# Kernel tuning notes

Hardware: AMD Instinct MI355X
Metric: run time of the kernel (lower is better)

The kernel has to match this reference:

```python
import jax, jax.numpy as jnp
import numpy as np

N, L, H, Q = 64, 258, 1024, 256
WINDOW = 16.0
DEV_POW = 128.0  # 2 * (window/2)^2, Luong local-p sigma = D/2


def setup_inputs() -> dict:
    key = jax.random.key(0)
    k1, k2, k3, k4, k5, k6 = jax.random.split(key, 6)
    encoder_outputs = jax.random.normal(k1, (N, L, H), dtype=jnp.float32)
    decoder_h_t = jax.random.normal(k2, (N, Q, H), dtype=jnp.float32)
    src_len = jax.random.randint(k3, (N,), 32, L + 1).astype(jnp.int32)
    # window centers within each source sentence
    p_t = jax.random.uniform(k4, (N,), dtype=jnp.float32) * (src_len.astype(jnp.float32) - 1.0)
    W_a = jax.random.normal(k5, (H, H), dtype=jnp.float32) * (1.0 / np.sqrt(H))
    W_c = jax.random.normal(k6, (H, 2 * H), dtype=jnp.float32) * (1.0 / np.sqrt(2 * H))
    return {"encoder_outputs": encoder_outputs, "decoder_h_t": decoder_h_t,
            "src_len": src_len, "p_t": p_t, "W_a": W_a, "W_c": W_c}


def reference(encoder_outputs, decoder_h_t, src_len, p_t, W_a, W_c):
    n, l, h = encoder_outputs.shape
    idx = jnp.arange(l, dtype=jnp.float32)  # index_matrix, length == max_length == L

    # local_p window: [p_t - D, p_t + D], clamped to [0, src_len]
    src_end = src_len.astype(jnp.float32)
    attn_start = jnp.maximum(p_t - WINDOW, 0.0)          # [N]
    attn_end = jnp.minimum(p_t + WINDOW, src_end)        # [N]
    mask = (idx[None, :] < attn_start[:, None]) | (idx[None, :] > attn_end[:, None])  # [N,L]

    # Luong 'general' score: h_t^T W_a h_s -> [N,Q,L]
    score = jnp.einsum('nqh,hk,nlk->nql', decoder_h_t, W_a, encoder_outputs)

    score = jnp.where(mask[:, None, :], -1e9, score)
    align = jax.nn.softmax(score, axis=2)                 # [N,Q,L]

    # gaussian reweighting centered at p_t
    gauss = jnp.exp(-((idx[None, :] - p_t[:, None]) ** 2) / DEV_POW)  # [N,L]
    align = align * gauss[:, None, :]

    context = jnp.einsum('nql,nlh->nqh', align, encoder_outputs)      # [N,Q,H]
    cat = jnp.concatenate([context, decoder_h_t], axis=2)             # [N,Q,2H]
    return jnp.tanh(cat @ W_c.T)                                      # [N,Q,H]
```

## Files before the change

kernel.cpp:

```cpp
#include <hip/hip_runtime.h>
#include <hip/hip_bf16.h>
#include <cstdint>

#define DEVINL __device__ __forceinline__

typedef __attribute__((ext_vector_type(8))) short short8;
typedef __attribute__((ext_vector_type(4))) float f32x4;
typedef __attribute__((ext_vector_type(4))) unsigned short u16x4;

static constexpr int NB = 64, LL = 258, HH = 1024, QQ = 256;
static constexpr int WROWS = 33;
static constexpr int MU = 2176;
static constexpr int VTN = 4096;

static constexpr size_t OFF_META = 0;
static constexpr size_t SZ_WE   = (size_t)MU * HH * 2;
static constexpr size_t OFF_WEHI = 1024;
static constexpr size_t OFF_WELO = OFF_WEHI + SZ_WE;
static constexpr size_t OFF_WAHI = OFF_WELO + SZ_WE;
static constexpr size_t OFF_WALO = OFF_WAHI + (size_t)HH * HH * 2;
static constexpr size_t OFF_WCBF = OFF_WALO + (size_t)HH * HH * 2;
static constexpr size_t OFF_HBF  = OFF_WCBF + (size_t)HH * 2 * HH * 2;
static constexpr size_t OFF_U    = OFF_HBF + (size_t)NB * QQ * HH * 2;
static constexpr size_t OFF_UHI  = OFF_U;
static constexpr size_t OFF_ULO  = OFF_U + (size_t)MU * HH * 2;
static constexpr size_t OFF_CTX  = OFF_U + (size_t)MU * HH * 4;
static constexpr size_t OFF_VT   = OFF_CTX + (size_t)NB * QQ * HH * 2;

DEVINL unsigned short f2bf(float x) {
    union { float f; uint32_t u; } v; v.f = x;
    uint32_t u = v.u;
    uint32_t r = (u + 0x7FFFu + ((u >> 16) & 1u)) >> 16;
    return (unsigned short)r;
}
DEVINL float bf2f(unsigned short b) {
    union { uint32_t u; float f; } v; v.u = ((uint32_t)b) << 16;
    return v.f;
}

template <typename T>
DEVINL void lds_load16(const T* g, T* l) {
    __builtin_amdgcn_global_load_lds(
        (const __attribute__((address_space(1))) void*)g,
        (__attribute__((address_space(3))) void*)l, 16, 0, 0);
}

DEVINL float fast_tanh(float x) {
    float e = __expf(2.0f * x);
    return 1.0f - 2.0f / (e + 1.0f);
}

DEVINL void window_of(float p, int sl, int& ls, int& lc) {
    float se = (float)sl;
    float s = fmaxf(p - 16.0f, 0.0f);
    float e = fminf(p + 16.0f, se);
    ls = (int)ceilf(s);
    int le = (int)floorf(e); if (le > LL - 1) le = LL - 1;
    lc = le - ls + 1;
    if (lc < 0) lc = 0;
    if (lc > WROWS) lc = WROWS;
}

__global__ __launch_bounds__(256) void k_prep(const float* __restrict__ enc,
                                              const float* __restrict__ ht,
                                              const float* __restrict__ pt,
                                              const int* __restrict__ slen,
                                              const float* __restrict__ Wa,
                                              const float* __restrict__ Wc,
                                              unsigned short* __restrict__ wehi,
                                              unsigned short* __restrict__ welo,
                                              unsigned short* __restrict__ wahi,
                                              unsigned short* __restrict__ walo,
                                              unsigned short* __restrict__ wcbf,
                                              unsigned short* __restrict__ hbf) {
    const int b = blockIdx.x, t = threadIdx.x;
    if (b < MU) {
        int r = b;
        const float* src = nullptr;
        bool valid = false;
        if (r < NB * WROWS) {
            int n = r / WROWS, li = r - n * WROWS;
            int ls, lc;
            window_of(pt[n], slen[n], ls, lc);
            if (li < lc) { valid = true; src = enc + ((size_t)n * LL + ls + li) * HH; }
        }
        f32x4 v;
        if (valid) v = ((const f32x4*)src)[t];
        else { v[0] = 0.f; v[1] = 0.f; v[2] = 0.f; v[3] = 0.f; }
        u16x4 h, l;
#pragma unroll
        for (int j = 0; j < 4; ++j) {
            unsigned short hb = f2bf(v[j]);
            h[j] = hb;
            l[j] = f2bf(v[j] - bf2f(hb));
        }
        size_t o = (size_t)r * HH / 4 + t;
        ((u16x4*)wehi)[o] = h;
        ((u16x4*)welo)[o] = l;
    } else if (b < MU + 1024) {
        int i = (b - MU) * 256 + t;
        f32x4 v = ((const f32x4*)Wa)[i];
        u16x4 h, l;
#pragma unroll
        for (int j = 0; j < 4; ++j) {
            unsigned short hb = f2bf(v[j]);
            h[j] = hb;
            l[j] = f2bf(v[j] - bf2f(hb));
        }
        ((u16x4*)wahi)[i] = h;
        ((u16x4*)walo)[i] = l;
    } else if (b < MU + 1024 + 2048) {
        int i = (b - MU - 1024) * 256 + t;
        f32x4 v = ((const f32x4*)Wc)[i];
        u16x4 h;
#pragma unroll
        for (int j = 0; j < 4; ++j) h[j] = f2bf(v[j]);
        ((u16x4*)wcbf)[i] = h;
    } else {
        int i = (b - MU - 3072) * 256 + t;
        f32x4 v = ((const f32x4*)ht)[i];
        u16x4 h;
#pragma unroll
        for (int j = 0; j < 4; ++j) h[j] = f2bf(v[j]);
        ((u16x4*)hbf)[i] = h;
    }
}

__global__ __launch_bounds__(256) void k_ugemm64(const unsigned short* __restrict__ Ahi,
                                                 const unsigned short* __restrict__ Alo,
                                                 const unsigned short* __restrict__ Bhi,
                                                 const unsigned short* __restrict__ Blo,
                                                 unsigned short* __restrict__ Uhi,
                                                 unsigned short* __restrict__ Ulo) {
    __shared__ unsigned short sAh[2][64 * 32], sAl[2][64 * 32], sBh[2][64 * 32], sBl[2][64 * 32];
    const int tid = threadIdx.x;
    const int w = tid >> 6, lane = tid & 63;
    const int m0 = blockIdx.y * 64, n0 = blockIdx.x * 64;
    const int wr = w >> 1, wc = w & 1;
    const int r16 = lane & 15, khalf = lane >> 4;
    const int srow = tid >> 2;
    const int scol = ((tid & 3) ^ ((tid >> 3) & 3)) * 8;
    const int ldso = tid * 8;
    const int kslot = (khalf ^ ((r16 >> 1) & 3)) * 8;
    f32x4 acc[2][2] = {};

    auto stage = [&](int buf, int kb) {
        lds_load16(Ahi + (size_t)(m0 + srow) * HH + kb + scol, &sAh[buf][ldso]);
        lds_load16(Alo + (size_t)(m0 + srow) * HH + kb + scol, &sAl[buf][ldso]);
        lds_load16(Bhi + (size_t)(n0 + srow) * HH + kb + scol, &sBh[buf][ldso]);
        lds_load16(Blo + (size_t)(n0 + srow) * HH + kb + scol, &sBl[buf][ldso]);
    };

    stage(0, 0);
    for (int t = 0; t < 32; ++t) {
        const int buf = t & 1;
        asm volatile("s_waitcnt vmcnt(0)" ::: "memory");
        __builtin_amdgcn_s_barrier();
        short8 ah[2], al[2], bh[2], bl[2];
#pragma unroll
        for (int f = 0; f < 2; ++f) {
            int ai = (wr * 32 + f * 16 + r16) * 32 + kslot;
            ah[f] = *(const short8*)&sAh[buf][ai];
            al[f] = *(const short8*)&sAl[buf][ai];
            int bi = (wc * 32 + f * 16 + r16) * 32 + kslot;
            bh[f] = *(const short8*)&sBh[buf][bi];
            bl[f] = *(const short8*)&sBl[buf][bi];
        }
        if (t + 1 < 32) stage(buf ^ 1, (t + 1) * 32);
        asm volatile("s_waitcnt lgkmcnt(0)" ::: "memory");
        __builtin_amdgcn_sched_barrier(0);
#pragma unroll
        for (int mf = 0; mf < 2; ++mf)
#pragma unroll
            for (int nf = 0; nf < 2; ++nf) {
                acc[mf][nf] = __builtin_amdgcn_mfma_f32_16x16x32_bf16(ah[mf], bh[nf], acc[mf][nf], 0, 0, 0);
                acc[mf][nf] = __builtin_amdgcn_mfma_f32_16x16x32_bf16(ah[mf], bl[nf], acc[mf][nf], 0, 0, 0);
                acc[mf][nf] = __builtin_amdgcn_mfma_f32_16x16x32_bf16(al[mf], bh[nf], acc[mf][nf], 0, 0, 0);
            }
        __builtin_amdgcn_s_barrier();
    }
    const int rg = lane >> 4;
#pragma unroll
    for (int mf = 0; mf < 2; ++mf)
#pragma unroll
        for (int nf = 0; nf < 2; ++nf)
#pragma unroll
            for (int r = 0; r < 4; ++r) {
                int m = m0 + wr * 32 + mf * 16 + rg * 4 + r;
                int nn = n0 + wc * 32 + nf * 16 + r16;
                float v = acc[mf][nf][r];
                unsigned short h = f2bf(v);
                Uhi[(size_t)m * HH + nn] = h;
                Ulo[(size_t)m * HH + nn] = f2bf(v - bf2f(h));
            }
}

__global__ __launch_bounds__(256) void k_vgemm64(const unsigned short* __restrict__ Wc1,
                                                 const unsigned short* __restrict__ Bhi,
                                                 const unsigned short* __restrict__ Blo,
                                                 unsigned short* __restrict__ VT) {
    __shared__ unsigned short sA[2][64 * 32], sBh[2][64 * 32], sBl[2][64 * 32];
    const int tid = threadIdx.x;
    const int w = tid >> 6, lane = tid & 63;
    const int m0 = blockIdx.y * 64, n0 = blockIdx.x * 64;
    const int wr = w >> 1, wc = w & 1;
    const int r16 = lane & 15, khalf = lane >> 4;
    const int srow = tid >> 2;
    const int scol = ((tid & 3) ^ ((tid >> 3) & 3)) * 8;
    const int ldso = tid * 8;
    const int kslot = (khalf ^ ((r16 >> 1) & 3)) * 8;
    f32x4 acc[2][2] = {};

    auto stage = [&](int buf, int kb) {
        lds_load16(Wc1 + (size_t)(m0 + srow) * (2 * HH) + kb + scol, &sA[buf][ldso]);
        lds_load16(Bhi + (size_t)(n0 + srow) * HH + kb + scol, &sBh[buf][ldso]);
        lds_load16(Blo + (size_t)(n0 + srow) * HH + kb + scol, &sBl[buf][ldso]);
    };

    stage(0, 0);
    for (int t = 0; t < 32; ++t) {
        const int buf = t & 1;
        asm volatile("s_waitcnt vmcnt(0)" ::: "memory");
        __builtin_amdgcn_s_barrier();
        short8 af[2], bh[2], bl[2];
#pragma unroll
        for (int f = 0; f < 2; ++f) {
            af[f] = *(const short8*)&sA[buf][(wr * 32 + f * 16 + r16) * 32 + kslot];
            int bi = (wc * 32 + f * 16 + r16) * 32 + kslot;
            bh[f] = *(const short8*)&sBh[buf][bi];
            bl[f] = *(const short8*)&sBl[buf][bi];
        }
        if (t + 1 < 32) stage(buf ^ 1, (t + 1) * 32);
        asm volatile("s_waitcnt lgkmcnt(0)" ::: "memory");
        __builtin_amdgcn_sched_barrier(0);
#pragma unroll
        for (int mf = 0; mf < 2; ++mf)
#pragma unroll
            for (int nf = 0; nf < 2; ++nf) {
                acc[mf][nf] = __builtin_amdgcn_mfma_f32_16x16x32_bf16(af[mf], bh[nf], acc[mf][nf], 0, 0, 0);
                acc[mf][nf] = __builtin_amdgcn_mfma_f32_16x16x32_bf16(af[mf], bl[nf], acc[mf][nf], 0, 0, 0);
            }
        __builtin_amdgcn_s_barrier();
    }
    const int rg = lane >> 4;
#pragma unroll
    for (int mf = 0; mf < 2; ++mf)
#pragma unroll
        for (int nf = 0; nf < 2; ++nf)
#pragma unroll
            for (int r = 0; r < 4; ++r) {
                int o = m0 + wr * 32 + mf * 16 + rg * 4 + r;
                int wrow = n0 + wc * 32 + nf * 16 + r16;
                int n = wrow / WROWS, li = wrow - n * WROWS;
                if (n < NB)
                    VT[(size_t)o * VTN + n * 64 + li] = f2bf(acc[mf][nf][r]);
            }
}

__global__ __launch_bounds__(256) void k_attn2(const float* __restrict__ ht,
                                               const unsigned short* __restrict__ Uhi,
                                               const unsigned short* __restrict__ Ulo,
                                               const unsigned short* __restrict__ VT,
                                               const float* __restrict__ pt,
                                               const int* __restrict__ slen,
                                               unsigned short* __restrict__ ctxP) {
    __shared__ float sPart[4][32 * 48];
    __shared__ float sScore[32 * 48];
    __shared__ unsigned short sPhi[32 * 72];
    __shared__ unsigned short sPlo[32 * 72];

    const int tid = threadIdx.x;
    const int w = tid >> 6, lane = tid & 63;
    const int n = blockIdx.x >> 3, q0 = (blockIdx.x & 7) * 32;
    int ls, lc;
    window_of(pt[n], slen[n], ls, lc);
    const float p = pt[n];
    const int r16 = lane & 15, khalf = lane >> 4, rg = lane >> 4;

    const float* hbase = ht + ((size_t)(n * QQ + q0)) * HH;
    const unsigned short* uhbase = Uhi + (size_t)n * WROWS * HH;
    const unsigned short* ulbase = Ulo + (size_t)n * WROWS * HH;

    f32x4 acc[2][3] = {};
    for (int ks = 0; ks < 8; ++ks) {
        int kcol = w * 256 + ks * 32 + khalf * 8;
        short8 ah[2], al[2];
#pragma unroll
        for (int mf = 0; mf < 2; ++mf) {
            const float* src = hbase + (size_t)(mf * 16 + r16) * HH + kcol;
            f32x4 v0 = *(const f32x4*)src;
            f32x4 v1 = *(const f32x4*)(src + 4);
            float vv[8] = {v0[0], v0[1], v0[2], v0[3], v1[0], v1[1], v1[2], v1[3]};
#pragma unroll
            for (int j = 0; j < 8; ++j) {
                unsigned short hb = f2bf(vv[j]);
                ah[mf][j] = (short)hb;
                al[mf][j] = (short)f2bf(vv[j] - bf2f(hb));
            }
        }
#pragma unroll
        for (int nf = 0; nf < 3; ++nf) {
            size_t uoff = (size_t)(nf * 16 + r16) * HH + kcol;
            short8 bh = *(const short8*)(uhbase + uoff);
            short8 bl = *(const short8*)(ulbase + uoff);
#pragma unroll
            for (int mf = 0; mf < 2; ++mf) {
                acc[mf][nf] = __builtin_amdgcn_mfma_f32_16x16x32_bf16(ah[mf], bh, acc[mf][nf], 0, 0, 0);
                acc[mf][nf] = __builtin_amdgcn_mfma_f32_16x16x32_bf16(ah[mf], bl, acc[mf][nf], 0, 0, 0);
                acc[mf][nf] = __builtin_amdgcn_mfma_f32_16x16x32_bf16(al[mf], bh, acc[mf][nf], 0, 0, 0);
            }
        }
    }
#pragma unroll
    for (int mf = 0; mf < 2; ++mf)
#pragma unroll
        for (int nf = 0; nf < 3; ++nf)
#pragma unroll
            for (int r = 0; r < 4; ++r)
                sPart[w][(mf * 16 + rg * 4 + r) * 48 + nf * 16 + r16] = acc[mf][nf][r];
    __syncthreads();

    {
        int q = tid >> 3, g = tid & 7;
        float sc6[6];
#pragma unroll
        for (int s = 0; s < 6; ++s) {
            int li = g + 8 * s;
            int o = q * 48 + li;
            sc6[s] = sPart[0][o] + sPart[1][o] + sPart[2][o] + sPart[3][o];
        }
        float mx = -1e30f;
#pragma unroll
        for (int s = 0; s < 6; ++s) { int li = g + 8 * s; if (li < lc) mx = fmaxf(mx, sc6[s]); }
        for (int off = 1; off < 8; off <<= 1) mx = fmaxf(mx, __shfl_xor(mx, off, 8));
        float sum = 0.f, ex[6];
#pragma unroll
        for (int s = 0; s < 6; ++s) {
            int li = g + 8 * s;
            float e = (li < lc) ? __expf(sc6[s] - mx) : 0.f;
            ex[s] = e; sum += e;
        }
        for (int off = 1; off < 8; off <<= 1) sum += __shfl_xor(sum, off, 8);
        float inv = 1.0f / sum;
#pragma unroll
        for (int s = 0; s < 6; ++s) {
            int li = g + 8 * s;
            float d = (float)(ls + li) - p;
            float gs = __expf(-(d * d) * (1.0f / 128.0f));
            sScore[q * 48 + li] = ex[s] * inv * gs;
        }
    }
    __syncthreads();

    {
        int row = tid >> 3, c0 = (tid & 7) * 8;
#pragma unroll
        for (int j = 0; j < 8; ++j) {
            int c = c0 + j;
            float pv = (c < 48) ? sScore[row * 48 + c] : 0.f;
            unsigned short hb = f2bf(pv);
            sPhi[row * 72 + c] = hb;
            sPlo[row * 72 + c] = f2bf(pv - bf2f(hb));
        }
    }
    __syncthreads();

    short8 pa[2][2], plq[2][2];
#pragma unroll
    for (int mf = 0; mf < 2; ++mf)
#pragma unroll
        for (int ks = 0; ks < 2; ++ks) {
            pa[mf][ks]  = *(const short8*)&sPhi[(mf * 16 + r16) * 72 + ks * 32 + khalf * 8];
            plq[mf][ks] = *(const short8*)&sPlo[(mf * 16 + r16) * 72 + ks * 32 + khalf * 8];
        }
    const unsigned short* vtb = VT + n * 64 + khalf * 8;
#pragma unroll
    for (int half = 0; half < 2; ++half) {
        f32x4 accB[2][8] = {};
        const int hcol0 = w * 256 + half * 128;
#pragma unroll
        for (int nf = 0; nf < 8; ++nf) {
            const int o = hcol0 + nf * 16 + r16;
#pragma unroll
            for (int ks = 0; ks < 2; ++ks) {
                short8 bfrag = *(const short8*)(vtb + (size_t)o * VTN + ks * 32);
#pragma unroll
                for (int mf = 0; mf < 2; ++mf) {
                    accB[mf][nf] = __builtin_amdgcn_mfma_f32_16x16x32_bf16(pa[mf][ks], bfrag, accB[mf][nf], 0, 0, 0);
                    accB[mf][nf] = __builtin_amdgcn_mfma_f32_16x16x32_bf16(plq[mf][ks], bfrag, accB[mf][nf], 0, 0, 0);
                }
            }
        }
        const int nt = w * 2 + half;
#pragma unroll
        for (int mf = 0; mf < 2; ++mf) {
            const int rb = q0 + mf * 16;
            const int mt = n * 2 + (rb >> 7);
            const int rowbit = (rb >> 6) & 1;
            const int mq = (rb >> 4) & 3;
#pragma unroll
            for (int pp = 0; pp < 4; ++pp) {
                short8 pk;
#pragma unroll
                for (int r = 0; r < 4; ++r) {
                    pk[r]     = (short)f2bf(accB[mf][2 * pp][r]);
                    pk[4 + r] = (short)f2bf(accB[mf][2 * pp + 1][r]);
                }
                const int widc = rowbit * 2 + (pp >> 1);
                const int fid = mq * 2 + (pp & 1);
                size_t off = ((((size_t)(mt * 8 + nt) * 4 + widc) * 8 + fid) * 64 + lane) * 8;
                *(short8*)&ctxP[off] = pk;
            }
        }
    }
}

__global__ __launch_bounds__(256) void k_out_gemm128(
    const unsigned short* __restrict__ Ahf,
    const unsigned short* __restrict__ Bt,
    const unsigned short* __restrict__ Cp,
    float* __restrict__ out) {
    __shared__ unsigned short sA[128 * 64], sB[128 * 64];

    const int tid = threadIdx.x;
    const int wid = tid >> 6, lane = tid & 63;
    const int bid = blockIdx.x;
    const int swz = (bid & 7) * 128 + (bid >> 3);
    const int mt = swz >> 3, nt = swz & 7;
    const int m0 = mt * 128, n0 = nt * 128;
    const int wr = wid >> 1, wc = wid & 1;
    const int r16 = lane & 15, kg = lane >> 4;

    const int srow8 = lane >> 3;
    const int kswz = ((lane & 7) ^ srow8) * 8;

    f32x4 acc[4][4] = {};

    for (int t = 0; t < 16; ++t) {
        const int kb = t * 64;
        if (t > 0) __syncthreads();
#pragma unroll
        for (int i = 0; i < 4; ++i) {
            int row = i * 32 + wid * 8 + srow8;
            lds_load16(Ahf + (size_t)(m0 + row) * HH + kb + kswz,
                       &sA[i * 2048 + wid * 512]);
            lds_load16(Bt + (size_t)(n0 + row) * (2 * HH) + 1024 + kb + kswz,
                       &sB[i * 2048 + wid * 512]);
        }
        asm volatile("s_waitcnt vmcnt(0)" ::: "memory");
        __syncthreads();

        short8 a[4][2];
#pragma unroll
        for (int mq = 0; mq < 4; ++mq)
#pragma unroll
            for (int ks = 0; ks < 2; ++ks)
                a[mq][ks] = *(const short8*)&sA[(wr * 64 + mq * 16 + r16) * 64 +
                                                (((ks * 4 + kg) ^ (r16 & 7)) * 8)];
#pragma unroll
        for (int nq = 0; nq < 4; ++nq) {
            short8 b0 = *(const short8*)&sB[(wc * 64 + nq * 16 + r16) * 64 +
                                            (((0 + kg) ^ (r16 & 7)) * 8)];
            short8 b1 = *(const short8*)&sB[(wc * 64 + nq * 16 + r16) * 64 +
                                            (((4 + kg) ^ (r16 & 7)) * 8)];
#pragma unroll
            for (int mq = 0; mq < 4; ++mq) {
                acc[mq][nq] = __builtin_amdgcn_mfma_f32_16x16x32_bf16(a[mq][0], b0, acc[mq][nq], 0, 0, 0);
                acc[mq][nq] = __builtin_amdgcn_mfma_f32_16x16x32_bf16(a[mq][1], b1, acc[mq][nq], 0, 0, 0);
            }
        }
    }

    const size_t cbase = (((size_t)(mt * 8 + nt) * 4 + wid) * 8) * 512 + (size_t)lane * 8;
    short8 cv[8];
#pragma unroll
    for (int f = 0; f < 8; ++f)
        cv[f] = *(const short8*)&Cp[cbase + (size_t)f * 512];
#pragma unroll
    for (int mq = 0; mq < 4; ++mq)
#pragma unroll
        for (int nq = 0; nq < 4; ++nq) {
            const int f = mq * 2 + (nq >> 1);
            const int part = (nq & 1) * 4;
            int row = m0 + wr * 64 + mq * 16 + kg * 4;
            int col = n0 + wc * 64 + nq * 16 + r16;
#pragma unroll
            for (int r = 0; r < 4; ++r) {
                float cadd = bf2f((unsigned short)cv[f][part + r]);
                out[(size_t)(row + r) * HH + col] = fast_tanh(acc[mq][nq][r] + cadd);
            }
        }
}

extern "C" void kernel_launch(void* const* d_in, const int* in_sizes, int n_in,
                              void* d_out, int out_size, void* d_ws, size_t ws_size,
                              hipStream_t stream) {
    const float* enc  = (const float*)d_in[0];
    const float* ht   = (const float*)d_in[1];
    const int*   slen = (const int*)d_in[2];
    const float* pt   = (const float*)d_in[3];
    const float* Wa   = (const float*)d_in[4];
    const float* Wc   = (const float*)d_in[5];
    float* out = (float*)d_out;

    char* ws = (char*)d_ws;
    unsigned short* wehi = (unsigned short*)(ws + OFF_WEHI);
    unsigned short* welo = (unsigned short*)(ws + OFF_WELO);
    unsigned short* wahi = (unsigned short*)(ws + OFF_WAHI);
    unsigned short* walo = (unsigned short*)(ws + OFF_WALO);
    unsigned short* wcbf = (unsigned short*)(ws + OFF_WCBF);
    unsigned short* hbf  = (unsigned short*)(ws + OFF_HBF);
    unsigned short* uhi  = (unsigned short*)(ws + OFF_UHI);
    unsigned short* ulo  = (unsigned short*)(ws + OFF_ULO);
    unsigned short* ctxP = (unsigned short*)(ws + OFF_CTX);
    unsigned short* vt   = (unsigned short*)(ws + OFF_VT);

    hipLaunchKernelGGL(k_prep, dim3(MU + 1024 + 2048 + 16384), dim3(256), 0, stream,
                       enc, ht, pt, slen, Wa, Wc, wehi, welo, wahi, walo, wcbf, hbf);
    hipLaunchKernelGGL(k_ugemm64, dim3(HH / 64, MU / 64), dim3(256), 0, stream,
                       wehi, welo, wahi, walo, uhi, ulo);
    hipLaunchKernelGGL(k_vgemm64, dim3(MU / 64, HH / 64), dim3(256), 0, stream,
                       wcbf, wehi, welo, vt);
    hipLaunchKernelGGL(k_attn2, dim3(NB * 8), dim3(256), 0, stream,
                       ht, uhi, ulo, vt, pt, slen, ctxP);
    hipLaunchKernelGGL(k_out_gemm128, dim3(1024), dim3(256), 0, stream,
                       hbf, wcbf, ctxP, out);
}
```

Baseline: 158.7 us.

## Merge U and V window GEMMs into one launch with 64x128 tiles

Fuses the two independent GEMMs (encoder-window times W_a, and W_c1 times encoder-window) into a single kernel whose blocks split by index into the two jobs. It also widens each block tile from 64x64 to 64x128 so each wave computes 2x4 fragments. The aim is to drop one launch and its tail, and to reuse the A tile across more output columns. In exchange, LDS per block grows to 48KB and the accumulator register count doubles, which may lower occupancy.

```diff
diff --git a/kernel.cpp b/kernel.cpp
--- a/kernel.cpp
+++ b/kernel.cpp
@@ -126,135 +126,142 @@
     }
 }
 
-__global__ __launch_bounds__(256) void k_ugemm64(const unsigned short* __restrict__ Ahi,
-                                                 const unsigned short* __restrict__ Alo,
-                                                 const unsigned short* __restrict__ Bhi,
-                                                 const unsigned short* __restrict__ Blo,
-                                                 unsigned short* __restrict__ Uhi,
-                                                 unsigned short* __restrict__ Ulo) {
-    __shared__ unsigned short sAh[2][64 * 32], sAl[2][64 * 32], sBh[2][64 * 32], sBl[2][64 * 32];
+__global__ __launch_bounds__(256) void k_wgemm(const unsigned short* __restrict__ wehi,
+                                               const unsigned short* __restrict__ welo,
+                                               const unsigned short* __restrict__ wahi,
+                                               const unsigned short* __restrict__ walo,
+                                               const unsigned short* __restrict__ wcbf,
+                                               unsigned short* __restrict__ Uhi,
+                                               unsigned short* __restrict__ Ulo,
+                                               unsigned short* __restrict__ VT) {
+    __shared__ unsigned short smem[24576];
     const int tid = threadIdx.x;
     const int w = tid >> 6, lane = tid & 63;
-    const int m0 = blockIdx.y * 64, n0 = blockIdx.x * 64;
     const int wr = w >> 1, wc = w & 1;
-    const int r16 = lane & 15, khalf = lane >> 4;
+    const int r16 = lane & 15, khalf = lane >> 4, rg = lane >> 4;
     const int srow = tid >> 2;
     const int scol = ((tid & 3) ^ ((tid >> 3) & 3)) * 8;
-    const int ldso = tid * 8;
     const int kslot = (khalf ^ ((r16 >> 1) & 3)) * 8;
-    f32x4 acc[2][2] = {};
-
-    auto stage = [&](int buf, int kb) {
-        lds_load16(Ahi + (size_t)(m0 + srow) * HH + kb + scol, &sAh[buf][ldso]);
-        lds_load16(Alo + (size_t)(m0 + srow) * HH + kb + scol, &sAl[buf][ldso]);
-        lds_load16(Bhi + (size_t)(n0 + srow) * HH + kb + scol, &sBh[buf][ldso]);
-        lds_load16(Blo + (size_t)(n0 + srow) * HH + kb + scol, &sBl[buf][ldso]);
-    };
-
-    stage(0, 0);
-    for (int t = 0; t < 32; ++t) {
-        const int buf = t & 1;
-        asm volatile("s_waitcnt vmcnt(0)" ::: "memory");
-        __builtin_amdgcn_s_barrier();
-        short8 ah[2], al[2], bh[2], bl[2];
-#pragma unroll
-        for (int f = 0; f < 2; ++f) {
-            int ai = (wr * 32 + f * 16 + r16) * 32 + kslot;
-            ah[f] = *(const short8*)&sAh[buf][ai];
-            al[f] = *(const short8*)&sAl[buf][ai];
-            int bi = (wc * 32 + f * 16 + r16) * 32 + kslot;
-            bh[f] = *(const short8*)&sBh[buf][bi];
-            bl[f] = *(const short8*)&sBl[buf][bi];
-        }
-        if (t + 1 < 32) stage(buf ^ 1, (t + 1) * 32);
-        asm volatile("s_waitcnt lgkmcnt(0)" ::: "memory");
-        __builtin_amdgcn_sched_barrier(0);
+    const int bid = blockIdx.x;
+
+    if (bid < 272) {
+        const int m0 = (bid >> 3) * 64;
+        const int n0 = (bid & 7) * 128;
+        f32x4 acc[2][4] = {};
+
+        auto stage = [&](int buf, int kb) {
+            lds_load16(wehi + (size_t)(m0 + srow) * HH + kb + scol, &smem[buf * 2048 + tid * 8]);
+            lds_load16(welo + (size_t)(m0 + srow) * HH + kb + scol, &smem[4096 + buf * 2048 + tid * 8]);
+#pragma unroll
+            for (int i = 0; i < 2; ++i) {
+                lds_load16(wahi + (size_t)(n0 + i * 64 + srow) * HH + kb + scol,
+                           &smem[8192 + buf * 4096 + i * 2048 + tid * 8]);
+                lds_load16(walo + (size_t)(n0 + i * 64 + srow) * HH + kb + scol,
+                           &smem[16384 + buf * 4096 + i * 2048 + tid * 8]);
+            }
+        };
+
+        stage(0, 0);
+        for (int t = 0; t < 32; ++t) {
+            const int buf = t & 1;
+            asm volatile("s_waitcnt vmcnt(0)" ::: "memory");
+            __builtin_amdgcn_s_barrier();
+            short8 ah[2], al[2], bh[4], bl[4];
+#pragma unroll
+            for (int f = 0; f < 2; ++f) {
+                int ai = buf * 2048 + (wr * 32 + f * 16 + r16) * 32 + kslot;
+                ah[f] = *(const short8*)&smem[ai];
+                al[f] = *(const short8*)&smem[4096 + ai];
+            }
+#pragma unroll
+            for (int nf = 0; nf < 4; ++nf) {
+                int bi = buf * 4096 + (wc * 64 + nf * 16 + r16) * 32 + kslot;
+                bh[nf] = *(const short8*)&smem[8192 + bi];
+                bl[nf] = *(const short8*)&smem[16384 + bi];
+            }
+            if (t + 1 < 32) stage(buf ^ 1, (t + 1) * 32);
+            asm volatile("s_waitcnt lgkmcnt(0)" ::: "memory");
+            __builtin_amdgcn_sched_barrier(0);
+#pragma unroll
+            for (int mf = 0; mf < 2; ++mf)
+#pragma unroll
+                for (int nf = 0; nf < 4; ++nf) {
+                    acc[mf][nf] = __builtin_amdgcn_mfma_f32_16x16x32_bf16(ah[mf], bh[nf], acc[mf][nf], 0, 0, 0);
+                    acc[mf][nf] = __builtin_amdgcn_mfma_f32_16x16x32_bf16(ah[mf], bl[nf], acc[mf][nf], 0, 0, 0);
+                    acc[mf][nf] = __builtin_amdgcn_mfma_f32_16x16x32_bf16(al[mf], bh[nf], acc[mf][nf], 0, 0, 0);
+                }
+            __builtin_amdgcn_s_barrier();
+        }
 #pragma unroll
         for (int mf = 0; mf < 2; ++mf)
 #pragma unroll
-            for (int nf = 0; nf < 2; ++nf) {
-                acc[mf][nf] = __builtin_amdgcn_mfma_f32_16x16x32_bf16(ah[mf], bh[nf], acc[mf][nf], 0, 0, 0);
-                acc[mf][nf] = __builtin_amdgcn_mfma_f32_16x16x32_bf16(ah[mf], bl[nf], acc[mf][nf], 0, 0, 0);
-                acc[mf][nf] = __builtin_amdgcn_mfma_f32_16x16x32_bf16(al[mf], bh[nf], acc[mf][nf], 0, 0, 0);
-            }
-        __builtin_amdgcn_s_barrier();
-    }
-    const int rg = lane >> 4;
-#pragma unroll
-    for (int mf = 0; mf < 2; ++mf)
-#pragma unroll
-        for (int nf = 0; nf < 2; ++nf)
-#pragma unroll
-            for (int r = 0; r < 4; ++r) {
-                int m = m0 + wr * 32 + mf * 16 + rg * 4 + r;
-                int nn = n0 + wc * 32 + nf * 16 + r16;
-                float v = acc[mf][nf][r];
-                unsigned short h = f2bf(v);
-                Uhi[(size_t)m * HH + nn] = h;
-                Ulo[(size_t)m * HH + nn] = f2bf(v - bf2f(h));
-            }
-}
-
-__global__ __launch_bounds__(256) void k_vgemm64(const unsigned short* __restrict__ Wc1,
-                                                 const unsigned short* __restrict__ Bhi,
-                                                 const unsigned short* __restrict__ Blo,
-                                                 unsigned short* __restrict__ VT) {
-    __shared__ unsigned short sA[2][64 * 32], sBh[2][64 * 32], sBl[2][64 * 32];
-    const int tid = threadIdx.x;
-    const int w = tid >> 6, lane = tid & 63;
-    const int m0 = blockIdx.y * 64, n0 = blockIdx.x * 64;
-    const int wr = w >> 1, wc = w & 1;
-    const int r16 = lane & 15, khalf = lane >> 4;
-    const int srow = tid >> 2;
-    const int scol = ((tid & 3) ^ ((tid >> 3) & 3)) * 8;
-    const int ldso = tid * 8;
-    const int kslot = (khalf ^ ((r16 >> 1) & 3)) * 8;
-    f32x4 acc[2][2] = {};
-
-    auto stage = [&](int buf, int kb) {
-        lds_load16(Wc1 + (size_t)(m0 + srow) * (2 * HH) + kb + scol, &sA[buf][ldso]);
-        lds_load16(Bhi + (size_t)(n0 + srow) * HH + kb + scol, &sBh[buf][ldso]);
-        lds_load16(Blo + (size_t)(n0 + srow) * HH + kb + scol, &sBl[buf][ldso]);
-    };
-
-    stage(0, 0);
-    for (int t = 0; t < 32; ++t) {
-        const int buf = t & 1;
-        asm volatile("s_waitcnt vmcnt(0)" ::: "memory");
-        __builtin_amdgcn_s_barrier();
-        short8 af[2], bh[2], bl[2];
-#pragma unroll
-        for (int f = 0; f < 2; ++f) {
-            af[f] = *(const short8*)&sA[buf][(wr * 32 + f * 16 + r16) * 32 + kslot];
-            int bi = (wc * 32 + f * 16 + r16) * 32 + kslot;
-            bh[f] = *(const short8*)&sBh[buf][bi];
-            bl[f] = *(const short8*)&sBl[buf][bi];
-        }
-        if (t + 1 < 32) stage(buf ^ 1, (t + 1) * 32);
-        asm volatile("s_waitcnt lgkmcnt(0)" ::: "memory");
-        __builtin_amdgcn_sched_barrier(0);
+            for (int nf = 0; nf < 4; ++nf)
+#pragma unroll
+                for (int r = 0; r < 4; ++r) {
+                    int m = m0 + wr * 32 + mf * 16 + rg * 4 + r;
+                    int nn = n0 + wc * 64 + nf * 16 + r16;
+                    float v = acc[mf][nf][r];
+                    unsigned short h = f2bf(v);
+                    Uhi[(size_t)m * HH + nn] = h;
+                    Ulo[(size_t)m * HH + nn] = f2bf(v - bf2f(h));
+                }
+    } else {
+        const int b2 = bid - 272;
+        const int m0 = (b2 / 17) * 64;
+        const int n0 = (b2 % 17) * 128;
+        f32x4 acc[2][4] = {};
+
+        auto stage = [&](int buf, int kb) {
+            lds_load16(wcbf + (size_t)(m0 + srow) * (2 * HH) + kb + scol, &smem[buf * 2048 + tid * 8]);
+#pragma unroll
+            for (int i = 0; i < 2; ++i) {
+                lds_load16(wehi + (size_t)(n0 + i * 64 + srow) * HH + kb + scol,
+                           &smem[8192 + buf * 4096 + i * 2048 + tid * 8]);
+                lds_load16(welo + (size_t)(n0 + i * 64 + srow) * HH + kb + scol,
+                           &smem[16384 + buf * 4096 + i * 2048 + tid * 8]);
+            }
+        };
+
+        stage(0, 0);
+        for (int t = 0; t < 32; ++t) {
+            const int buf = t & 1;
+            asm volatile("s_waitcnt vmcnt(0)" ::: "memory");
+            __builtin_amdgcn_s_barrier();
+            short8 af[2], bh[4], bl[4];
+#pragma unroll
+            for (int f = 0; f < 2; ++f)
+                af[f] = *(const short8*)&smem[buf * 2048 + (wr * 32 + f * 16 + r16) * 32 + kslot];
+#pragma unroll
+            for (int nf = 0; nf < 4; ++nf) {
+                int bi = buf * 4096 + (wc * 64 + nf * 16 + r16) * 32 + kslot;
+                bh[nf] = *(const short8*)&smem[8192 + bi];
+                bl[nf] = *(const short8*)&smem[16384 + bi];
+            }
+            if (t + 1 < 32) stage(buf ^ 1, (t + 1) * 32);
+            asm volatile("s_waitcnt lgkmcnt(0)" ::: "memory");
+            __builtin_amdgcn_sched_barrier(0);
+#pragma unroll
+            for (int mf = 0; mf < 2; ++mf)
+#pragma unroll
+                for (int nf = 0; nf < 4; ++nf) {
+                    acc[mf][nf] = __builtin_amdgcn_mfma_f32_16x16x32_bf16(af[mf], bh[nf], acc[mf][nf], 0, 0, 0);
+                    acc[mf][nf] = __builtin_amdgcn_mfma_f32_16x16x32_bf16(af[mf], bl[nf], acc[mf][nf], 0, 0, 0);
+                }
+            __builtin_amdgcn_s_barrier();
+        }
 #pragma unroll
         for (int mf = 0; mf < 2; ++mf)
 #pragma unroll
-            for (int nf = 0; nf < 2; ++nf) {
-                acc[mf][nf] = __builtin_amdgcn_mfma_f32_16x16x32_bf16(af[mf], bh[nf], acc[mf][nf], 0, 0, 0);
-                acc[mf][nf] = __builtin_amdgcn_mfma_f32_16x16x32_bf16(af[mf], bl[nf], acc[mf][nf], 0, 0, 0);
-            }
-        __builtin_amdgcn_s_barrier();
-    }
-    const int rg = lane >> 4;
-#pragma unroll
-    for (int mf = 0; mf < 2; ++mf)
-#pragma unroll
-        for (int nf = 0; nf < 2; ++nf)
-#pragma unroll
-            for (int r = 0; r < 4; ++r) {
-                int o = m0 + wr * 32 + mf * 16 + rg * 4 + r;
-                int wrow = n0 + wc * 32 + nf * 16 + r16;
-                int n = wrow / WROWS, li = wrow - n * WROWS;
-                if (n < NB)
-                    VT[(size_t)o * VTN + n * 64 + li] = f2bf(acc[mf][nf][r]);
-            }
+            for (int nf = 0; nf < 4; ++nf)
+#pragma unroll
+                for (int r = 0; r < 4; ++r) {
+                    int o = m0 + wr * 32 + mf * 16 + rg * 4 + r;
+                    int wrow = n0 + wc * 64 + nf * 16 + r16;
+                    int n = wrow / WROWS, li = wrow - n * WROWS;
+                    if (n < NB)
+                        VT[(size_t)o * VTN + n * 64 + li] = f2bf(acc[mf][nf][r]);
+                }
+    }
 }
 
 __global__ __launch_bounds__(256) void k_attn2(const float* __restrict__ ht,
@@ -517,10 +524,8 @@
 
     hipLaunchKernelGGL(k_prep, dim3(MU + 1024 + 2048 + 16384), dim3(256), 0, stream,
                        enc, ht, pt, slen, Wa, Wc, wehi, welo, wahi, walo, wcbf, hbf);
-    hipLaunchKernelGGL(k_ugemm64, dim3(HH / 64, MU / 64), dim3(256), 0, stream,
-                       wehi, welo, wahi, walo, uhi, ulo);
-    hipLaunchKernelGGL(k_vgemm64, dim3(MU / 64, HH / 64), dim3(256), 0, stream,
-                       wcbf, wehi, welo, vt);
+    hipLaunchKernelGGL(k_wgemm, dim3(544), dim3(256), 0, stream,
+                       wehi, welo, wahi, walo, wcbf, uhi, ulo, vt);
     hipLaunchKernelGGL(k_attn2, dim3(NB * 8), dim3(256), 0, stream,
                        ht, uhi, ulo, vt, pt, slen, ctxP);
     hipLaunchKernelGGL(k_out_gemm128, dim3(1024), dim3(256), 0, stream,
```

After: 153.3 us. 3.5% less time.
